# Optimization experiments

Hardware: AMD Instinct MI355X
Metric: run time of the kernel (lower is better)

Reference implementation:

```python
import jax, jax.numpy as jnp
import numpy as np
import math

B = 1024
G = 34  # grid_dim = 17*2
C = 4
SCENT = 19


def _scent_kernel_np():
    h = w = SCENT
    mx, my = 0.5 * h, 0.5 * w
    sx, sy = h / 4.0, w / 4.0
    x = np.linspace(0.0, h, h)
    y = np.linspace(0.0, w, w)
    X, Y = np.meshgrid(x, y, indexing='ij')
    z = (1.0 / (2.0 * math.pi * sx * sy)) * np.exp(-(((X - mx) ** 2) / (2 * sx ** 2) + ((Y - my) ** 2) / (2 * sy ** 2)))
    return (z * 80.0).astype(np.float32)


def setup_inputs() -> dict:
    key = jax.random.key(0)
    k1, k2, k3, k4 = jax.random.split(key, 4)
    cell = jax.random.uniform(k1, (B, C, G, G), dtype=jnp.float32)
    food = (jax.random.uniform(k2, (B, G, G), dtype=jnp.float32) > 0.97).astype(jnp.float32)
    fc1_w = jax.random.normal(k3, (64, 12), dtype=jnp.float32) * (1.0 / np.sqrt(12))
    fc1_b = jnp.zeros((64,), dtype=jnp.float32)
    fc2_w = jax.random.normal(k4, (4, 64), dtype=jnp.float32) * (1.0 / np.sqrt(64))
    fc2_b = jnp.zeros((4,), dtype=jnp.float32)
    scent_kernel = jnp.asarray(_scent_kernel_np())
    return {"cell": cell, "food": food, "fc1_w": fc1_w, "fc1_b": fc1_b,
            "fc2_w": fc2_w, "fc2_b": fc2_b, "scent_kernel": scent_kernel, "steps": 32}


def _conv(x, w, pad, groups):
    # x: [B, Cin, H, W], w: [Cout, Cin/groups, kh, kw]; cross-correlation like torch
    return jax.lax.conv_general_dilated(
        x, w, window_strides=(1, 1), padding=[(pad, pad), (pad, pad)],
        feature_group_count=groups, dimension_numbers=('NCHW', 'OIHW', 'NCHW'))


def _maxpool3(x):
    # 3x3 max pool, stride 1, pad 1 (pad value -inf, matching torch MaxPool2d semantics)
    return jax.lax.reduce_window(x, -jnp.inf, jax.lax.max, (1, 1, 3, 3), (1, 1, 1, 1),
                                 [(0, 0), (0, 0), (1, 1), (1, 1)])


def _forward(cell, food, fc1_w, fc1_b, fc2_w, fc2_b, scent_kernel, steps):
    dx = jnp.outer(jnp.array([1., 2., 1.], jnp.float32), jnp.array([-1., 0., 1.], jnp.float32)) / 8.0
    dy = dx.T
    kdx = jnp.tile(dx[None, None], (4, 1, 1, 1))  # depthwise, groups=4
    kdy = jnp.tile(dy[None, None], (4, 1, 1, 1))

    # perceive_scent: 19x19 gaussian conv, padding 9
    scent = _conv(food[:, None], scent_kernel[None, None], 9, 1)[:, 0]  # [B,G,G]

    def step(cell, _):
        cell = cell.at[:, 3].set(scent)
        # current living count per batch (cells in channel 0 above 0.8)
        cl = jnp.sum((cell[:, 0] > 0.8).astype(jnp.float32), axis=(1, 2))
        pre_mask = _maxpool3(cell[:, 0:1]) > 0.1  # [B,1,G,G]
        # perception: x, sobel-x, sobel-y -> 12 channels
        y1 = _conv(cell, kdx, 1, 4)
        y2 = _conv(cell, kdy, 1, 4)
        y = jnp.concatenate([cell, y1, y2], axis=1)  # [B,12,G,G]
        # tiny MLP per pixel (torch transposes dims 1<->3; linear over channels is equivalent)
        h = jax.nn.relu(jnp.einsum('bchw,oc->bohw', y, fc1_w) + fc1_b[None, :, None, None])
        upd = jnp.einsum('bchw,oc->bohw', h, fc2_w) + fc2_b[None, :, None, None]
        x = cell + upd
        post_mask = _maxpool3(x[:, 0:1]) > 0.1
        x = x * (pre_mask & post_mask).astype(x.dtype)
        x = jnp.clip(x, -10.0, 10.0)
        x = x.at[:, 0].set(jnp.clip(x[:, 0], 0.0, 1.0))
        # keep_k_largest: threshold = cl-th smallest (ascending sort index == cl); keep strictly greater
        flat = x[:, 0].reshape(B, -1)  # [B, G*G]
        srt = jnp.sort(flat, axis=1)
        kth = jnp.take_along_axis(srt, cl.astype(jnp.int32)[:, None], axis=1)  # [B,1] (gather clamps OOB)
        flat = jnp.where(flat > kth, flat, 0.0)
        x = x.at[:, 0].set(flat.reshape(B, G, G))
        return x, None

    cell, _ = jax.lax.scan(jax.checkpoint(step), cell, None, length=steps)
    total_pixel_val = cell[:, 0:1].sum(axis=(1, 2, 3))
    living_count = jnp.sum((cell[:, 0:1] > 0.1).astype(jnp.float32), axis=(1, 2, 3))
    return cell, food, total_pixel_val, living_count


def reference(cell, food, fc1_w, fc1_b, fc2_w, fc2_b, scent_kernel, steps):
    return _forward(cell, food, fc1_w, fc1_b, fc2_w, fc2_b, scent_kernel, steps)
```

## Files before the change

### kernel.cpp

```cpp
#include <hip/hip_runtime.h>
#include <stdint.h>

#define GD    34
#define GP    36
#define NPIX  1156
#define NT    512
#define NW    8
#define NB    1024
#define TPR   12
#define TUSED 408
#define SP    3

#define SCAN_PASS(KK) do {                                                         \
    if (wid == 0) {                                                                \
      const int base2 = lane << 4;                                                 \
      int c16[16]; int csum = 0;                                                   \
      _Pragma("unroll")                                                            \
      for (int j = 0; j < 16; ++j) { c16[j] = hist[base2+j]; hist[base2+j] = 0; csum += c16[j]; } \
      int inc = csum;                                                              \
      _Pragma("unroll")                                                            \
      for (int off2 = 1; off2 < 64; off2 <<= 1) { int vv = __shfl_up(inc, off2); if (lane >= off2) inc += vv; } \
      const int excl = inc - csum;                                                 \
      if ((KK) >= excl && (KK) < inc) {                                            \
        int rem = (KK) - excl; int cum = 0;                                        \
        _Pragma("unroll")                                                          \
        for (int j = 0; j < 16; ++j) {                                             \
          if (rem >= cum && rem < cum + c16[j]) { sel_bin = base2 + j; sel_rem = rem - cum; } \
          cum += c16[j];                                                           \
        }                                                                          \
      }                                                                            \
    }                                                                              \
  } while (0)

#define SN 7216

__global__ void pack_w(const float* __restrict__ fc1_w, const float* __restrict__ fc1_b,
                       const float* __restrict__ fc2_w, float* __restrict__ wp) {
  int o = threadIdx.x;
  if (o < 64) {
#pragma unroll
    for (int j = 0; j < 12; ++j) wp[o*20+j] = fc1_w[o*12+j];
    wp[o*20+12] = fc1_b[o];
    wp[o*20+13] = fc2_w[o];
    wp[o*20+14] = fc2_w[64+o];
    wp[o*20+15] = fc2_w[128+o];
    wp[o*20+16] = fc2_w[192+o];
  }
}

__global__ __launch_bounds__(NT) __attribute__((amdgpu_waves_per_eu(4, 8)))
void ca_kernel(const float* __restrict__ cell_in,
               const float* __restrict__ food_in,
               const float* __restrict__ fc2_b,
               const float* __restrict__ sk_g,
               const int*   __restrict__ steps_p,
               const float* __restrict__ wp,
               float* __restrict__ out)
{
  __shared__ float cbuf[3][GP*GP];
  __shared__ float S[SN];
  __shared__ int   mcount;
  __shared__ int   icl[2][NW];
  __shared__ int   inzaz[NW];
  __shared__ int   sel_bin, sel_rem;
  __shared__ float fsum[NW];
  __shared__ int   lcnt[NW];

  float* x0buf  = S;
  float* scentb = S + 1296;
  float* x1s    = S + 2592;
  float* x2s    = S + 3748;
  float* x3s    = S + 4904;
  int*   listpb = (int*)(S + 6060);
  int*   hist   = (int*)(S + 2592);

  const int tid  = threadIdx.x;
  const int b    = blockIdx.x;
  const int lane = tid & 63;
  const int wid  = tid >> 6;
  const int nsteps = steps_p[0];

  const bool tval = (tid < TUSED);
  const int  trow = tval ? (tid / TPR) : 0;
  const int  c0   = tval ? ((tid % TPR) * SP) : 0;
  const int  nval = tval ? ((c0 <= 31) ? 3 : 1) : 0;
  const int  pb0  = tval ? ((trow+1)*GP + c0 + 1) : 37;
  const int  p0   = trow*GD + c0;

  const int r0b = pb0 - (c0 + 1);
  const int rm1 = r0b - GP, rp1 = r0b + GP;
  const int rm2 = (r0b - 2*GP < 0) ? 0 : (r0b - 2*GP);
  const int rp2 = (r0b + 2*GP > 35*GP) ? 35*GP : (r0b + 2*GP);

  for (int idx = tid; idx < 3*GP*GP; idx += NT) (&cbuf[0][0])[idx] = 0.f;
  for (int idx = tid; idx < SN;      idx += NT) S[idx] = 0.f;
  if (tid == 0) mcount = 0;
  __syncthreads();

  float v3k[SP];
  int cnt0 = 0;
#pragma unroll
  for (int j = 0; j < SP; ++j) {
    v3k[j] = 0.f;
    if (j < nval) {
      int p = p0 + j;
      const float* gi = cell_in + (size_t)b*4*NPIX + p;
      float v0 = gi[0], v1 = gi[NPIX], v2 = gi[2*NPIX], v3 = gi[3*NPIX];
      cbuf[0][pb0+j] = v0; cbuf[1][pb0+j] = v1; cbuf[2][pb0+j] = v2;
      v3k[j] = v3;
      cnt0 += (v0 > 0.8f) ? 1 : 0;
      S[(trow+9)*52 + (c0+j+9)] = food_in[(size_t)b*NPIX + p];
    }
  }
#pragma unroll
  for (int off = 32; off; off >>= 1) cnt0 += __shfl_down(cnt0, off);
  if (lane == 0) icl[0][wid] = cnt0;
  __syncthreads();

  float scent[SP];
#pragma unroll
  for (int j = 0; j < SP; ++j) {
    float ssum = 0.f;
    if (j < nval) {
      for (int dr = 0; dr < 19; ++dr) {
        const float* frow = S + (trow+dr)*52 + (c0+j);
        const float* krow = sk_g + dr*19;
#pragma unroll
        for (int dc = 0; dc < 19; ++dc) ssum = fmaf(frow[dc], krow[dc], ssum);
      }
    }
    scent[j] = ssum;
  }
  __syncthreads();
  for (int idx = tid; idx < SN; idx += NT) S[idx] = 0.f;
  __syncthreads();
#pragma unroll
  for (int j = 0; j < SP; ++j) if (j < nval) scentb[pb0+j] = scent[j];

  const float b2r0 = fc2_b[0], b2r1 = fc2_b[1], b2r2 = fc2_b[2], b2r3 = fc2_b[3];

  for (int s = 0; s < nsteps; ++s) {
    __syncthreads();
    float cm3[7], cm5[7];
#pragma unroll
    for (int jc = 0; jc < 7; ++jc) {
      cm3[jc] = 0.f; cm5[jc] = 0.f;
      if (jc < nval + 4) {
        int pc = c0 - 1 + jc;
        pc = (pc < 0) ? 0 : ((pc > 35) ? 35 : pc);
        const float* cb = cbuf[0];
        float c3 = fmaxf(fmaxf(cb[rm1+pc], cb[r0b+pc]), cb[rp1+pc]);
        cm3[jc] = c3;
        cm5[jc] = fmaxf(fmaxf(cb[rm2+pc], cb[rp2+pc]), c3);
      }
    }
    unsigned pm = 0;
    int act[SP];
#pragma unroll
    for (int j = 0; j < SP; ++j) {
      if (j < nval && fmaxf(fmaxf(cm3[j+1], cm3[j+2]), cm3[j+3]) > 0.1f) pm |= (1u << j);
      float a5 = fmaxf(fmaxf(fmaxf(cm5[j], cm5[j+1]), fmaxf(cm5[j+2], cm5[j+3])), cm5[j+4]);
      act[j] = (j < nval) && (a5 > 0.1f);
    }
    int nloc = act[0] + act[1] + act[2];
    int inc = nloc;
#pragma unroll
    for (int off = 1; off < 64; off <<= 1) { int v = __shfl_up(inc, off); if (lane >= off) inc += v; }
    const int excl = inc - nloc;
    const int wtot = __shfl(inc, 63);
    int woff = 0;
    if (lane == 63) woff = atomicAdd(&mcount, wtot);
    woff = __shfl(woff, 63);
    int myo = woff + excl;
#pragma unroll
    for (int j = 0; j < SP; ++j)
      if (act[j]) listpb[myo++] = (pb0 + j) | ((p0 + j) << 16);
    __syncthreads();
    const int totm = mcount;
    for (int base = 0; base < totm; base += NT) {
      const int gi = base + tid;
      if (gi < totm) {
        const int e  = listpb[gi];
        const int pb = e & 0xffff;
        const int p  = e >> 16;
        float y0,y1,y2,y3,y4,y5,y6,y7,y8,y9,y10,y11;
        {
          const float* cb = cbuf[0];
          float t00=cb[pb-GP-1], t01=cb[pb-GP], t02=cb[pb-GP+1];
          float t10=cb[pb-1],    t11=cb[pb],    t12=cb[pb+1];
          float t20=cb[pb+GP-1], t21=cb[pb+GP], t22=cb[pb+GP+1];
          y0 = t11;
          y4 = ((t02 - t00) + 2.f*(t12 - t10) + (t22 - t20)) * 0.125f;
          y8 = ((t20 - t00) + 2.f*(t21 - t01) + (t22 - t02)) * 0.125f;
        }
        {
          const float* cb = cbuf[1];
          float t00=cb[pb-GP-1], t01=cb[pb-GP], t02=cb[pb-GP+1];
          float t10=cb[pb-1],    t11=cb[pb],    t12=cb[pb+1];
          float t20=cb[pb+GP-1], t21=cb[pb+GP], t22=cb[pb+GP+1];
          y1 = t11;
          y5 = ((t02 - t00) + 2.f*(t12 - t10) + (t22 - t20)) * 0.125f;
          y9 = ((t20 - t00) + 2.f*(t21 - t01) + (t22 - t02)) * 0.125f;
        }
        {
          const float* cb = cbuf[2];
          float t00=cb[pb-GP-1], t01=cb[pb-GP], t02=cb[pb-GP+1];
          float t10=cb[pb-1],    t11=cb[pb],    t12=cb[pb+1];
          float t20=cb[pb+GP-1], t21=cb[pb+GP], t22=cb[pb+GP+1];
          y2 = t11;
          y6 = ((t02 - t00) + 2.f*(t12 - t10) + (t22 - t20)) * 0.125f;
          y10= ((t20 - t00) + 2.f*(t21 - t01) + (t22 - t02)) * 0.125f;
        }
        {
          const float* cb = scentb;
          float t00=cb[pb-GP-1], t01=cb[pb-GP], t02=cb[pb-GP+1];
          float t10=cb[pb-1],    t11=cb[pb],    t12=cb[pb+1];
          float t20=cb[pb+GP-1], t21=cb[pb+GP], t22=cb[pb+GP+1];
          y3 = t11;
          y7 = ((t02 - t00) + 2.f*(t12 - t10) + (t22 - t20)) * 0.125f;
          y11= ((t20 - t00) + 2.f*(t21 - t01) + (t22 - t02)) * 0.125f;
        }
        float u0 = b2r0, u1 = b2r1, u2 = b2r2, u3 = b2r3;
        for (int o = 0; o < 64; ++o) {
          const float* wr = wp + o*20;
          float t = wr[12];
          t = fmaf(y0, wr[0], t);  t = fmaf(y1, wr[1], t);
          t = fmaf(y2, wr[2], t);  t = fmaf(y3, wr[3], t);
          t = fmaf(y4, wr[4], t);  t = fmaf(y5, wr[5], t);
          t = fmaf(y6, wr[6], t);  t = fmaf(y7, wr[7], t);
          t = fmaf(y8, wr[8], t);  t = fmaf(y9, wr[9], t);
          t = fmaf(y10, wr[10], t); t = fmaf(y11, wr[11], t);
          t = fmaxf(t, 0.f);
          u0 = fmaf(t, wr[13], u0);
          u1 = fmaf(t, wr[14], u1);
          u2 = fmaf(t, wr[15], u2);
          u3 = fmaf(t, wr[16], u3);
        }
        x0buf[pb] = y0 + u0;
        x1s[p]    = y1 + u1;
        x2s[p]    = y2 + u2;
        x3s[p]    = y3 + u3;
      }
    }
    __syncthreads();
    if (tid == 0) mcount = 0;
    unsigned pq = 0;
    float midv[SP];
#pragma unroll
    for (int j = 0; j < SP; ++j) midv[j] = 0.f;
    if (pm) {
      float dm[SP+2];
#pragma unroll
      for (int jc = 0; jc < SP+2; ++jc) {
        dm[jc] = 0.f;
        if (jc < nval + 2) {
          const int a = pb0 - 1 + jc;
          float u = x0buf[a-GP], m = x0buf[a], d = x0buf[a+GP];
          dm[jc] = fmaxf(fmaxf(u, m), d);
          if (jc >= 1 && jc <= nval) midv[jc-1] = m;
        }
      }
#pragma unroll
      for (int j = 0; j < SP; ++j)
        if (fmaxf(fmaxf(dm[j], dm[j+1]), dm[j+2]) > 0.1f) pq |= (1u << j);
    }
    int packed = 0;
    float v0s[SP];
#pragma unroll
    for (int j = 0; j < SP; ++j) {
      v0s[j] = 0.f;
      if (j < nval) {
        bool alive = ((pm >> j) & 1u) && ((pq >> j) & 1u);
        float v0 = 0.f, v1 = 0.f, v2 = 0.f, v3 = 0.f;
        if (alive) {
          v0 = fminf(fmaxf(midv[j],     0.f),  1.f);
          v1 = fminf(fmaxf(x1s[p0+j], -10.f), 10.f);
          v2 = fminf(fmaxf(x2s[p0+j], -10.f), 10.f);
          v3 = fminf(fmaxf(x3s[p0+j], -10.f), 10.f);
        }
        cbuf[1][pb0+j] = v1; cbuf[2][pb0+j] = v2; v3k[j] = v3;
        v0s[j] = v0;
        int zer = (v0 == 0.f) ? 1 : 0;
        int azf = (zer && v1 == 0.f && v2 == 0.f && v3 == 0.f) ? 1 : 0;
        packed += zer + (azf << 16);
      }
    }
#pragma unroll
    for (int off = 32; off; off >>= 1) packed += __shfl_down(packed, off);
    if (lane == 0) inzaz[wid] = packed;
    __syncthreads();
    int t01 = 0, cl = 0;
#pragma unroll
    for (int w = 0; w < NW; ++w) { t01 += inzaz[w]; cl += icl[s&1][w]; }
    const int nz = t01 & 0xffff, az = t01 >> 16;
    const int k  = (cl < NPIX) ? cl : (NPIX-1);
    float kth = 0.f;
    if (k >= nz) {
      hist[tid] = 0; hist[tid+512] = 0;
      __syncthreads();
      const int k2 = k - nz;
#pragma unroll
      for (int j = 0; j < SP; ++j) {
        unsigned u = __float_as_uint(v0s[j]);
        if (j < nval && u != 0u) atomicAdd(&hist[u >> 20], 1);
      }
      __syncthreads();
      SCAN_PASS(k2);
      __syncthreads();
      const int bin1 = sel_bin; const int kr2 = sel_rem;
#pragma unroll
      for (int j = 0; j < SP; ++j) {
        unsigned u = __float_as_uint(v0s[j]);
        if (j < nval && u != 0u && (u >> 20) == (unsigned)bin1)
          atomicAdd(&hist[(u >> 10) & 1023u], 1);
      }
      __syncthreads();
      SCAN_PASS(kr2);
      __syncthreads();
      const int bin2 = sel_bin; const int kr3 = sel_rem;
      const unsigned pref2 = (((unsigned)bin1) << 10) | (unsigned)bin2;
#pragma unroll
      for (int j = 0; j < SP; ++j) {
        unsigned u = __float_as_uint(v0s[j]);
        if (j < nval && u != 0u && (u >> 10) == pref2)
          atomicAdd(&hist[u & 1023u], 1);
      }
      __syncthreads();
      SCAN_PASS(kr3);
      __syncthreads();
      kth = __uint_as_float((((unsigned)bin1) << 20) | (((unsigned)bin2) << 10) | (unsigned)sel_bin);
    }
    int cnt = 0;
#pragma unroll
    for (int j = 0; j < SP; ++j) {
      if (j < nval) {
        float w0 = (v0s[j] > kth) ? v0s[j] : 0.f;
        cbuf[0][pb0+j] = w0;
        cnt += (w0 > 0.8f) ? 1 : 0;
      }
    }
#pragma unroll
    for (int off = 32; off; off >>= 1) cnt += __shfl_down(cnt, off);
    if (lane == 0) icl[(s+1)&1][wid] = cnt;
    if (az == NPIX) break;
  }

  const size_t CELL_N = (size_t)4*NPIX*NB;
  const size_t FOOD_N = (size_t)NPIX*NB;
  float tp = 0.f; int lcv = 0;
#pragma unroll
  for (int j = 0; j < SP; ++j) {
    if (j < nval) {
      const int p = p0 + j;
      float c0v = cbuf[0][pb0+j], c1 = cbuf[1][pb0+j], c2 = cbuf[2][pb0+j];
      size_t go = (size_t)b*4*NPIX + p;
      out[go]          = c0v;
      out[go +   NPIX] = c1;
      out[go + 2*NPIX] = c2;
      out[go + 3*NPIX] = v3k[j];
      out[CELL_N + (size_t)b*NPIX + p] = food_in[(size_t)b*NPIX + p];
      tp += c0v;
      lcv += (c0v > 0.1f) ? 1 : 0;
    }
  }
#pragma unroll
  for (int off = 32; off; off >>= 1) { tp += __shfl_down(tp, off); lcv += __shfl_down(lcv, off); }
  if (lane == 0) { fsum[wid] = tp; lcnt[wid] = lcv; }
  __syncthreads();
  if (tid == 0) {
    float tps = 0.f; int lcs = 0;
#pragma unroll
    for (int w = 0; w < NW; ++w) { tps += fsum[w]; lcs += lcnt[w]; }
    out[CELL_N + FOOD_N + b]      = tps;
    out[CELL_N + FOOD_N + NB + b] = (float)lcs;
  }
}

extern "C" void kernel_launch(void* const* d_in, const int* in_sizes, int n_in,
                              void* d_out, int out_size, void* d_ws, size_t ws_size,
                              hipStream_t stream) {
  const float* cell  = (const float*)d_in[0];
  const float* food  = (const float*)d_in[1];
  const float* fc1w  = (const float*)d_in[2];
  const float* fc1b  = (const float*)d_in[3];
  const float* fc2w  = (const float*)d_in[4];
  const float* fc2b  = (const float*)d_in[5];
  const float* sk    = (const float*)d_in[6];
  const int*   steps = (const int*)d_in[7];
  float* out = (float*)d_out;
  float* wp  = (float*)d_ws;
  pack_w<<<1, 64, 0, stream>>>(fc1w, fc1b, fc2w, wp);
  ca_kernel<<<NB, NT, 0, stream>>>(cell, food, fc2b, sk, steps, wp, out);
}
```

Before: 270.8 us.

## Process two active pixels per thread in MLP to reuse weight loads; alias list buffer

Rewrites the active-pixel MLP loop. Each thread reads up to three list entries into registers, then the buffer is released with a barrier, so the list can share space with x1s/hist and shared memory shrinks. When there are more active pixels than threads, each thread evaluates two pixels together so every weight load from global memory feeds two FMAs, and a third pixel is handled on its own. The cost is more registers, which may lower occupancy, and the list is capped at three entries per thread.

```diff
diff --git a/kernel.cpp b/kernel.cpp
--- a/kernel.cpp
+++ b/kernel.cpp
@@ -32,7 +32,38 @@
     }                                                                              \
   } while (0)
 
-#define SN 7216
+#define G9(CBP, PB, YC, YSX, YSY) do {                                             \
+    const float* cb_ = (CBP);                                                      \
+    float t00=cb_[(PB)-GP-1], t01=cb_[(PB)-GP], t02=cb_[(PB)-GP+1];                \
+    float t10=cb_[(PB)-1],    t11=cb_[(PB)],    t12=cb_[(PB)+1];                   \
+    float t20=cb_[(PB)+GP-1], t21=cb_[(PB)+GP], t22=cb_[(PB)+GP+1];                \
+    (YC)  = t11;                                                                   \
+    (YSX) = ((t02 - t00) + 2.f*(t12 - t10) + (t22 - t20)) * 0.125f;                \
+    (YSY) = ((t20 - t00) + 2.f*(t21 - t01) + (t22 - t02)) * 0.125f;                \
+  } while (0)
+
+#define MLP_ONE(EV) do {                                                           \
+    const int pb_ = (EV) & 0xffff; const int p_ = (EV) >> 16;                      \
+    float Y[12];                                                                   \
+    G9(cbuf[0], pb_, Y[0], Y[4], Y[8]);                                            \
+    G9(cbuf[1], pb_, Y[1], Y[5], Y[9]);                                            \
+    G9(cbuf[2], pb_, Y[2], Y[6], Y[10]);                                           \
+    G9(scentb,  pb_, Y[3], Y[7], Y[11]);                                           \
+    float u0 = b2r0, u1 = b2r1, u2 = b2r2, u3 = b2r3;                              \
+    for (int o = 0; o < 64; ++o) {                                                 \
+      const float* wr = wp + o*20;                                                 \
+      float t = wr[12];                                                            \
+      _Pragma("unroll")                                                            \
+      for (int k_ = 0; k_ < 12; ++k_) t = fmaf(Y[k_], wr[k_], t);                  \
+      t = fmaxf(t, 0.f);                                                           \
+      u0 = fmaf(t, wr[13], u0); u1 = fmaf(t, wr[14], u1);                          \
+      u2 = fmaf(t, wr[15], u2); u3 = fmaf(t, wr[16], u3);                          \
+    }                                                                              \
+    x0buf[pb_] = Y[0] + u0; x1s[p_] = Y[1] + u1;                                   \
+    x2s[p_]    = Y[2] + u2; x3s[p_] = Y[3] + u3;                                   \
+  } while (0)
+
+#define SN 6060
 
 __global__ void pack_w(const float* __restrict__ fc1_w, const float* __restrict__ fc1_b,
                        const float* __restrict__ fc2_w, float* __restrict__ wp) {
@@ -71,7 +102,7 @@
   float* x1s    = S + 2592;
   float* x2s    = S + 3748;
   float* x3s    = S + 4904;
-  int*   listpb = (int*)(S + 6060);
+  int*   listpb = (int*)(S + 2592);
   int*   hist   = (int*)(S + 2592);
 
   const int tid  = threadIdx.x;
@@ -177,73 +208,51 @@
       if (act[j]) listpb[myo++] = (pb0 + j) | ((p0 + j) << 16);
     __syncthreads();
     const int totm = mcount;
-    for (int base = 0; base < totm; base += NT) {
-      const int gi = base + tid;
-      if (gi < totm) {
-        const int e  = listpb[gi];
-        const int pb = e & 0xffff;
-        const int p  = e >> 16;
-        float y0,y1,y2,y3,y4,y5,y6,y7,y8,y9,y10,y11;
-        {
-          const float* cb = cbuf[0];
-          float t00=cb[pb-GP-1], t01=cb[pb-GP], t02=cb[pb-GP+1];
-          float t10=cb[pb-1],    t11=cb[pb],    t12=cb[pb+1];
-          float t20=cb[pb+GP-1], t21=cb[pb+GP], t22=cb[pb+GP+1];
-          y0 = t11;
-          y4 = ((t02 - t00) + 2.f*(t12 - t10) + (t22 - t20)) * 0.125f;
-          y8 = ((t20 - t00) + 2.f*(t21 - t01) + (t22 - t02)) * 0.125f;
-        }
-        {
-          const float* cb = cbuf[1];
-          float t00=cb[pb-GP-1], t01=cb[pb-GP], t02=cb[pb-GP+1];
-          float t10=cb[pb-1],    t11=cb[pb],    t12=cb[pb+1];
-          float t20=cb[pb+GP-1], t21=cb[pb+GP], t22=cb[pb+GP+1];
-          y1 = t11;
-          y5 = ((t02 - t00) + 2.f*(t12 - t10) + (t22 - t20)) * 0.125f;
-          y9 = ((t20 - t00) + 2.f*(t21 - t01) + (t22 - t02)) * 0.125f;
-        }
-        {
-          const float* cb = cbuf[2];
-          float t00=cb[pb-GP-1], t01=cb[pb-GP], t02=cb[pb-GP+1];
-          float t10=cb[pb-1],    t11=cb[pb],    t12=cb[pb+1];
-          float t20=cb[pb+GP-1], t21=cb[pb+GP], t22=cb[pb+GP+1];
-          y2 = t11;
-          y6 = ((t02 - t00) + 2.f*(t12 - t10) + (t22 - t20)) * 0.125f;
-          y10= ((t20 - t00) + 2.f*(t21 - t01) + (t22 - t02)) * 0.125f;
-        }
-        {
-          const float* cb = scentb;
-          float t00=cb[pb-GP-1], t01=cb[pb-GP], t02=cb[pb-GP+1];
-          float t10=cb[pb-1],    t11=cb[pb],    t12=cb[pb+1];
-          float t20=cb[pb+GP-1], t21=cb[pb+GP], t22=cb[pb+GP+1];
-          y3 = t11;
-          y7 = ((t02 - t00) + 2.f*(t12 - t10) + (t22 - t20)) * 0.125f;
-          y11= ((t20 - t00) + 2.f*(t21 - t01) + (t22 - t02)) * 0.125f;
-        }
-        float u0 = b2r0, u1 = b2r1, u2 = b2r2, u3 = b2r3;
+    int e0 = -1, e1 = -1, e2 = -1;
+    if (tid < totm)        e0 = listpb[tid];
+    if (NT + tid < totm)   e1 = listpb[NT + tid];
+    if (2*NT + tid < totm) e2 = listpb[2*NT + tid];
+    __syncthreads();
+    if (tid == 0) mcount = 0;
+    if (totm <= NT) {
+      if (e0 >= 0) MLP_ONE(e0);
+    } else {
+      {
+        const int pba = e0 & 0xffff; const int pa = e0 >> 16;
+        const bool vb = (e1 >= 0);
+        const int pbb = vb ? (e1 & 0xffff) : 37;
+        const int pb2 = vb ? (e1 >> 16) : 0;
+        float Ya[12], Yb[12];
+        G9(cbuf[0], pba, Ya[0], Ya[4], Ya[8]);   G9(cbuf[0], pbb, Yb[0], Yb[4], Yb[8]);
+        G9(cbuf[1], pba, Ya[1], Ya[5], Ya[9]);   G9(cbuf[1], pbb, Yb[1], Yb[5], Yb[9]);
+        G9(cbuf[2], pba, Ya[2], Ya[6], Ya[10]);  G9(cbuf[2], pbb, Yb[2], Yb[6], Yb[10]);
+        G9(scentb,  pba, Ya[3], Ya[7], Ya[11]);  G9(scentb,  pbb, Yb[3], Yb[7], Yb[11]);
+        float ua0 = b2r0, ua1 = b2r1, ua2 = b2r2, ua3 = b2r3;
+        float ub0 = b2r0, ub1 = b2r1, ub2 = b2r2, ub3 = b2r3;
         for (int o = 0; o < 64; ++o) {
           const float* wr = wp + o*20;
-          float t = wr[12];
-          t = fmaf(y0, wr[0], t);  t = fmaf(y1, wr[1], t);
-          t = fmaf(y2, wr[2], t);  t = fmaf(y3, wr[3], t);
-          t = fmaf(y4, wr[4], t);  t = fmaf(y5, wr[5], t);
-          t = fmaf(y6, wr[6], t);  t = fmaf(y7, wr[7], t);
-          t = fmaf(y8, wr[8], t);  t = fmaf(y9, wr[9], t);
-          t = fmaf(y10, wr[10], t); t = fmaf(y11, wr[11], t);
-          t = fmaxf(t, 0.f);
-          u0 = fmaf(t, wr[13], u0);
-          u1 = fmaf(t, wr[14], u1);
-          u2 = fmaf(t, wr[15], u2);
-          u3 = fmaf(t, wr[16], u3);
+          float ta = wr[12], tb = wr[12];
+#pragma unroll
+          for (int k = 0; k < 12; ++k) {
+            ta = fmaf(Ya[k], wr[k], ta);
+            tb = fmaf(Yb[k], wr[k], tb);
+          }
+          ta = fmaxf(ta, 0.f); tb = fmaxf(tb, 0.f);
+          ua0 = fmaf(ta, wr[13], ua0); ub0 = fmaf(tb, wr[13], ub0);
+          ua1 = fmaf(ta, wr[14], ua1); ub1 = fmaf(tb, wr[14], ub1);
+          ua2 = fmaf(ta, wr[15], ua2); ub2 = fmaf(tb, wr[15], ub2);
+          ua3 = fmaf(ta, wr[16], ua3); ub3 = fmaf(tb, wr[16], ub3);
         }
-        x0buf[pb] = y0 + u0;
-        x1s[p]    = y1 + u1;
-        x2s[p]    = y2 + u2;
-        x3s[p]    = y3 + u3;
-      }
+        x0buf[pba] = Ya[0] + ua0; x1s[pa] = Ya[1] + ua1;
+        x2s[pa]    = Ya[2] + ua2; x3s[pa] = Ya[3] + ua3;
+        if (vb) {
+          x0buf[pbb] = Yb[0] + ub0; x1s[pb2] = Yb[1] + ub1;
+          x2s[pb2]   = Yb[2] + ub2; x3s[pb2] = Yb[3] + ub3;
+        }
+      }
+      if (e2 >= 0) MLP_ONE(e2);
     }
     __syncthreads();
-    if (tid == 0) mcount = 0;
     unsigned pq = 0;
     float midv[SP];
 #pragma unroll
```

After: 270.4 us. About the same (-0.1%).
